# Kernel optimization log

Measured on AMD Instinct MI355X. Metric: run time of the kernel, lower is better.

Reference implementation:

```python
import jax, jax.numpy as jnp
import numpy as np

N_HEADS = 16


def _apply_rope(x, rope):
    # x: [B, H, N, Dh], rope: [B, N, Dh]; consecutive (even, odd) pairs form complex numbers
    xr, xi = x[..., 0::2], x[..., 1::2]              # [B,H,N,Dh/2]
    rr, ri = rope[:, None, :, 0::2], rope[:, None, :, 1::2]  # [B,1,N,Dh/2]
    or_ = xr * rr - xi * ri
    oi = xr * ri + xi * rr
    return jnp.stack([or_, oi], axis=-1).reshape(x.shape)


def setup_inputs() -> dict:
    key = jax.random.key(0)
    ks = jax.random.split(key, 8)
    B, N, D, Dh = 2, 2048, 2048, 128
    s = 0.02
    return {
        "x": jax.random.normal(ks[0], (B, N, D), jnp.float32),
        "q_rope": jax.random.normal(ks[1], (B, N, Dh), jnp.float32),
        "k_rope": jax.random.normal(ks[2], (B, N, Dh), jnp.float32),
        "Wq": jax.random.normal(ks[3], (D, D), jnp.float32) * s,
        "Wk": jax.random.normal(ks[4], (D, D), jnp.float32) * s,
        "Wv": jax.random.normal(ks[5], (D, D), jnp.float32) * s,
        "Wo": jax.random.normal(ks[6], (D, D), jnp.float32) * s,
        "bo": jax.random.normal(ks[7], (D,), jnp.float32) * s,
    }


def reference(x, q_rope, k_rope, Wq, Wk, Wv, Wo, bo):
    B, N, D = x.shape
    H = N_HEADS
    Dh = D // H
    # QKV projections (weights stored as [in, out])
    q = (x @ Wq).reshape(B, N, H, Dh).transpose(0, 2, 1, 3)  # [B,H,N,Dh]
    k = (x @ Wk).reshape(B, N, H, Dh).transpose(0, 2, 1, 3)
    v = (x @ Wv).reshape(B, N, H, Dh).transpose(0, 2, 1, 3)
    # NOTE: original scales q by d_head^-0.5 AND F.sdpa applies its default
    # 1/sqrt(d_head) scale again -> total score scale 1/d_head (faithful).
    q = q * (Dh ** -0.5)
    q = _apply_rope(q, q_rope)
    k = _apply_rope(k, k_rope)
    scores = jnp.einsum('bhnd,bhmd->bhnm', q, k) * (Dh ** -0.5)
    attn = jax.nn.softmax(scores, axis=-1)
    out = jnp.einsum('bhnm,bhmd->bhnd', attn, v)  # [B,H,N,Dh]
    out = out.transpose(0, 2, 1, 3).reshape(B, N, D)
    return out @ Wo + bo
```

## Files before the change

kernel.cpp:

```cpp
#include <hip/hip_runtime.h>
#include <hip/hip_bf16.h>
#include <stdint.h>


typedef __attribute__((ext_vector_type(4))) float f32x4;
typedef __attribute__((ext_vector_type(8))) short bf16x8;

__device__ __forceinline__ unsigned short f2bf(float f){
  unsigned u = __builtin_bit_cast(unsigned, f);
  u += 0x7FFFu + ((u >> 16) & 1u);
  return (unsigned short)(u >> 16);
}
__device__ __forceinline__ float bf2f(unsigned short h){
  unsigned u = ((unsigned)h) << 16;
  return __builtin_bit_cast(float, u);
}
__device__ __forceinline__ void gload16(const void* g, void* l){
  __builtin_amdgcn_global_load_lds((const __attribute__((address_space(1))) void*)g,
                                   (__attribute__((address_space(3))) void*)l, 16, 0, 0);
}

__global__ void k_cvt(const float* __restrict__ src, unsigned short* __restrict__ dst, int n4){
  int i = blockIdx.x * 256 + threadIdx.x;
  if (i >= n4) return;
  float4 v = ((const float4*)src)[i];
  unsigned long long pk = (unsigned long long)f2bf(v.x)
    | ((unsigned long long)f2bf(v.y) << 16)
    | ((unsigned long long)f2bf(v.z) << 32)
    | ((unsigned long long)f2bf(v.w) << 48);
  ((unsigned long long*)dst)[i] = pk;
}

__global__ void k_transpose_w(const float* __restrict__ W, unsigned short* __restrict__ WT){
  __shared__ float tile[64][65];
  int t = threadIdx.x;
  int cc = t & 63, rb = t >> 6;
  int bx = blockIdx.x * 64;
  int by = blockIdx.y * 64;
  #pragma unroll
  for (int i = 0; i < 16; i++){
    int r = rb + i * 4;
    tile[r][cc] = W[(size_t)(by + r) * 2048 + bx + cc];
  }
  __syncthreads();
  #pragma unroll
  for (int i = 0; i < 16; i++){
    int r = rb + i * 4;
    WT[(size_t)(bx + r) * 2048 + by + cc] = f2bf(tile[cc][r]);
  }
}

__global__ __launch_bounds__(256, 3) void k_gemm_qkv(
    const unsigned short* __restrict__ A,
    const unsigned short* __restrict__ Bt,
    unsigned short* __restrict__ Oq,
    unsigned short* __restrict__ Ok,
    unsigned short* __restrict__ Ov,
    const float* __restrict__ ropeq,
    const float* __restrict__ ropek)
{
  const int Kdim = 2048;
  __shared__ unsigned short As[128 * 64];
  __shared__ unsigned short Bs[128 * 64];
  const int tid = threadIdx.x;
  const int w = tid >> 6, l = tid & 63, g = l >> 4, c = l & 15;
  const int bm = blockIdx.x * 128, bn = blockIdx.y * 128;
  const int mw = (w >> 1) * 64, nw = (w & 1) * 64;
  f32x4 acc[4][4] = {};
  const int srow = l >> 3;
  const int sbyte = (((l & 7) ^ srow) << 4);
  const char* Ab = (const char*)A;
  const char* Bb = (const char*)Bt;
  char* AsB = (char*)As; char* BsB = (char*)Bs;

  for (int kt = 0; kt < Kdim; kt += 64){
    __syncthreads();
    #pragma unroll
    for (int j = 0; j < 4; j++){
      int chunk = w * 4 + j;
      int row = chunk * 8 + srow;
      gload16(Ab + ((size_t)(bm + row) * Kdim + kt) * 2 + sbyte, AsB + chunk * 1024);
      gload16(Bb + ((size_t)(bn + row) * Kdim + kt) * 2 + sbyte, BsB + chunk * 1024);
    }
    __syncthreads();
    #pragma unroll
    for (int kk = 0; kk < 2; kk++){
      bf16x8 av[4], bv[4];
      #pragma unroll
      for (int i = 0; i < 4; i++){
        int m = mw + i * 16 + c;
        av[i] = *(const bf16x8*)(AsB + m * 128 + ((kk * 64 + g * 16) ^ ((m & 7) << 4)));
        int n = nw + i * 16 + c;
        bv[i] = *(const bf16x8*)(BsB + n * 128 + ((kk * 64 + g * 16) ^ ((n & 7) << 4)));
      }
      #pragma unroll
      for (int i = 0; i < 4; i++)
        #pragma unroll
        for (int jj = 0; jj < 4; jj++)
          acc[i][jj] = __builtin_amdgcn_mfma_f32_16x16x32_bf16(av[i], bv[jj], acc[i][jj], 0, 0, 0);
    }
  }

  const int matsel = bn >> 11;
  const int hh = (bn >> 7) & 15;
  if (matsel < 2){
    unsigned short* O = matsel ? Ok : Oq;
    const float* rope = matsel ? ropek : ropeq;
    const float scale = matsel ? 1.0f : (1.0f / 128.0f);
    #pragma unroll
    for (int i = 0; i < 4; i++){
      int m0 = bm + mw + i * 16 + g * 4;
      #pragma unroll
      for (int jj = 0; jj < 4; jj++){
        int d = nw + jj * 16 + c;
        int dbase = d & ~1;
        int odd = d & 1;
        #pragma unroll
        for (int r = 0; r < 4; r++){
          int m = m0 + r;
          int b = m >> 11, tok = m & 2047;
          float v = acc[i][jj][r];
          float vp = __shfl_xor(v, 1);
          float2 rv = *(const float2*)(rope + (((size_t)(b * 2048 + tok)) << 7) + dbase);
          float xr = odd ? vp : v;
          float xi = odd ? v : vp;
          float res = odd ? (xr * rv.y + xi * rv.x) : (xr * rv.x - xi * rv.y);
          O[(((size_t)(b * 16 + hh) * 2048 + tok) << 7) + d] = f2bf(res * scale);
        }
      }
    }
  } else {
    #pragma unroll
    for (int i = 0; i < 4; i++){
      int m0 = bm + mw + i * 16 + g * 4;
      int b = m0 >> 11, tok0 = m0 & 2047;
      #pragma unroll
      for (int jj = 0; jj < 4; jj++){
        int d = nw + jj * 16 + c;
        unsigned long long pk = (unsigned long long)f2bf(acc[i][jj][0])
          | ((unsigned long long)f2bf(acc[i][jj][1]) << 16)
          | ((unsigned long long)f2bf(acc[i][jj][2]) << 32)
          | ((unsigned long long)f2bf(acc[i][jj][3]) << 48);
        *(unsigned long long*)(Ov + ((size_t)(b * 16 + hh) * 128 + d) * 2048 + tok0) = pk;
      }
    }
  }
}

__global__ __launch_bounds__(256, 3) void k_gemm_out(
    const unsigned short* __restrict__ A,
    const unsigned short* __restrict__ Bt,
    float* __restrict__ O,
    const float* __restrict__ bias)
{
  const int Kdim = 2048;
  __shared__ unsigned short As[128 * 64];
  __shared__ unsigned short Bs[128 * 64];
  const int tid = threadIdx.x;
  const int w = tid >> 6, l = tid & 63, g = l >> 4, c = l & 15;
  const int bm = blockIdx.x * 128, bn = blockIdx.y * 128;
  const int mw = (w >> 1) * 64, nw = (w & 1) * 64;
  f32x4 acc[4][4] = {};
  const int srow = l >> 3;
  const int sbyte = (((l & 7) ^ srow) << 4);
  const char* Ab = (const char*)A;
  const char* Bb = (const char*)Bt;
  char* AsB = (char*)As; char* BsB = (char*)Bs;

  for (int kt = 0; kt < Kdim; kt += 64){
    __syncthreads();
    #pragma unroll
    for (int j = 0; j < 4; j++){
      int chunk = w * 4 + j;
      int row = chunk * 8 + srow;
      gload16(Ab + ((size_t)(bm + row) * Kdim + kt) * 2 + sbyte, AsB + chunk * 1024);
      gload16(Bb + ((size_t)(bn + row) * Kdim + kt) * 2 + sbyte, BsB + chunk * 1024);
    }
    __syncthreads();
    #pragma unroll
    for (int kk = 0; kk < 2; kk++){
      bf16x8 av[4], bv[4];
      #pragma unroll
      for (int i = 0; i < 4; i++){
        int m = mw + i * 16 + c;
        av[i] = *(const bf16x8*)(AsB + m * 128 + ((kk * 64 + g * 16) ^ ((m & 7) << 4)));
        int n = nw + i * 16 + c;
        bv[i] = *(const bf16x8*)(BsB + n * 128 + ((kk * 64 + g * 16) ^ ((n & 7) << 4)));
      }
      #pragma unroll
      for (int i = 0; i < 4; i++)
        #pragma unroll
        for (int jj = 0; jj < 4; jj++)
          acc[i][jj] = __builtin_amdgcn_mfma_f32_16x16x32_bf16(av[i], bv[jj], acc[i][jj], 0, 0, 0);
    }
  }
  #pragma unroll
  for (int i = 0; i < 4; i++){
    int m0 = bm + mw + i * 16 + g * 4;
    #pragma unroll
    for (int jj = 0; jj < 4; jj++){
      int n = bn + nw + jj * 16 + c;
      float bv2 = bias[n];
      #pragma unroll
      for (int r = 0; r < 4; r++)
        O[(size_t)(m0 + r) * 2048 + n] = acc[i][jj][r] + bv2;
    }
  }
}

__global__ __launch_bounds__(256, 2) void k_attn(
    const unsigned short* __restrict__ Q,
    const unsigned short* __restrict__ Kg,
    const unsigned short* __restrict__ VT,
    unsigned short* __restrict__ Ao)
{
  __shared__ char sh[81920];
  char* PsB = sh + 65536;
  const int tid = threadIdx.x;
  const int w = tid >> 6, l = tid & 63, g = l >> 4, c = l & 15;
  const int qt = blockIdx.x, bh = blockIdx.y;
  const char* Qb = (const char*)(Q + (((size_t)bh * 2048 + qt * 128) << 7));
  const char* Kb = (const char*)(Kg + ((size_t)bh << 18));
  const char* Vb = (const char*)(VT + ((size_t)bh << 18));
  const int rsub = l >> 4;
  const int byte0 = (l & 15) << 4;
  const int drow = l >> 3;
  const int vbyte = (((l & 7) ^ drow) << 4);

  #pragma unroll
  for (int j = 0; j < 8; j++){
    int chunk = w * 8 + j;
    int row = chunk * 4 + rsub;
    gload16(Qb + (size_t)row * 256 + (byte0 ^ ((row & 7) << 4)), sh + chunk * 1024);
  }
  __syncthreads();
  bf16x8 qa[4][2];
  #pragma unroll
  for (int kk = 0; kk < 4; kk++)
    #pragma unroll
    for (int mf = 0; mf < 2; mf++){
      int q = w * 32 + mf * 16 + c;
      qa[kk][mf] = *(const bf16x8*)(sh + q * 256 + ((kk * 64 + g * 16) ^ ((q & 7) << 4)));
    }
  __syncthreads();

  auto stageKV = [&](int kv, int buf){
    char* Kc = sh + buf * 16384;
    char* Vc = sh + 32768 + buf * 16384;
    #pragma unroll
    for (int j = 0; j < 4; j++){
      int chunk = w * 4 + j;
      int row = chunk * 4 + rsub;
      gload16(Kb + (size_t)(kv * 64 + row) * 256 + (byte0 ^ ((row & 7) << 4)), Kc + chunk * 1024);
    }
    #pragma unroll
    for (int j = 0; j < 4; j++){
      int chunk = w * 4 + j;
      int d = chunk * 8 + drow;
      gload16(Vb + (size_t)d * 4096 + kv * 128 + vbyte, Vc + chunk * 1024);
    }
  };

  f32x4 oacc[2][8] = {};
  float lpart[2][4] = {};

  stageKV(0, 0);
  __syncthreads();

  for (int kv = 0; kv < 32; kv++){
    int cur = kv & 1;
    if (kv < 31) stageKV(kv + 1, cur ^ 1);
    char* Kc = sh + cur * 16384;
    char* Vc = sh + 32768 + cur * 16384;

    f32x4 sacc[2][4] = {};
    #pragma unroll
    for (int kk = 0; kk < 4; kk++){
      bf16x8 kbf[4];
      #pragma unroll
      for (int nf = 0; nf < 4; nf++){
        int kx = nf * 16 + c;
        kbf[nf] = *(const bf16x8*)(Kc + kx * 256 + ((kk * 64 + g * 16) ^ ((kx & 7) << 4)));
      }
      #pragma unroll
      for (int mf = 0; mf < 2; mf++)
        #pragma unroll
        for (int nf = 0; nf < 4; nf++)
          sacc[mf][nf] = __builtin_amdgcn_mfma_f32_16x16x32_bf16(qa[kk][mf], kbf[nf], sacc[mf][nf], 0, 0, 0);
    }

    #pragma unroll
    for (int mf = 0; mf < 2; mf++)
      #pragma unroll
      for (int nf = 0; nf < 4; nf++)
        #pragma unroll
        for (int r = 0; r < 4; r++){
          float pv = __expf(sacc[mf][nf][r]);
          sacc[mf][nf][r] = pv;
          lpart[mf][r] += pv;
        }

    #pragma unroll
    for (int mf = 0; mf < 2; mf++)
      #pragma unroll
      for (int nf = 0; nf < 4; nf++)
        #pragma unroll
        for (int r = 0; r < 4; r++){
          int q = w * 32 + mf * 16 + g * 4 + r;
          int key = nf * 16 + c;
          *(unsigned short*)(PsB + q * 128 + ((key * 2) ^ (((q >> 2) & 3) << 5))) = f2bf(sacc[mf][nf][r]);
        }
    __syncthreads();

    #pragma unroll
    for (int kk = 0; kk < 2; kk++){
      bf16x8 pa[2], vv[8];
      #pragma unroll
      for (int mf = 0; mf < 2; mf++){
        int q = w * 32 + mf * 16 + c;
        pa[mf] = *(const bf16x8*)(PsB + q * 128 + ((kk * 64 + g * 16) ^ (((q >> 2) & 3) << 5)));
      }
      #pragma unroll
      for (int df = 0; df < 8; df++){
        int d = df * 16 + c;
        vv[df] = *(const bf16x8*)(Vc + d * 128 + ((kk * 64 + g * 16) ^ ((d & 7) << 4)));
      }
      #pragma unroll
      for (int mf = 0; mf < 2; mf++)
        #pragma unroll
        for (int df = 0; df < 8; df++)
          oacc[mf][df] = __builtin_amdgcn_mfma_f32_16x16x32_bf16(pa[mf], vv[df], oacc[mf][df], 0, 0, 0);
    }
    __syncthreads();
  }

  int b = bh >> 4, h = bh & 15;
  #pragma unroll
  for (int mf = 0; mf < 2; mf++)
    #pragma unroll
    for (int r = 0; r < 4; r++){
      float s = lpart[mf][r];
      #pragma unroll
      for (int off = 1; off < 16; off <<= 1) s += __shfl_xor(s, off);
      float inv = 1.f / s;
      int qg = qt * 128 + w * 32 + mf * 16 + g * 4 + r;
      size_t rowbase = ((size_t)(b * 2048 + qg)) * 2048 + h * 128;
      #pragma unroll
      for (int df = 0; df < 8; df++)
        Ao[rowbase + df * 16 + c] = f2bf(oacc[mf][df][r] * inv);
    }
}

extern "C" void kernel_launch(void* const* d_in, const int* in_sizes, int n_in,
                              void* d_out, int out_size, void* d_ws, size_t ws_size,
                              hipStream_t stream){
  const float* x      = (const float*)d_in[0];
  const float* q_rope = (const float*)d_in[1];
  const float* k_rope = (const float*)d_in[2];
  const float* Wq     = (const float*)d_in[3];
  const float* Wk     = (const float*)d_in[4];
  const float* Wv     = (const float*)d_in[5];
  const float* Wo     = (const float*)d_in[6];
  const float* bo     = (const float*)d_in[7];
  char* ws = (char*)d_ws;
  unsigned short* xb  = (unsigned short*)(ws);
  unsigned short* wqT = (unsigned short*)(ws + 16777216);
  unsigned short* wkT = (unsigned short*)(ws + 25165824);
  unsigned short* wvT = (unsigned short*)(ws + 33554432);
  unsigned short* woT = (unsigned short*)(ws + 41943040);
  unsigned short* qb  = (unsigned short*)(ws + 50331648);
  unsigned short* kbf = (unsigned short*)(ws + 67108864);
  unsigned short* vt  = (unsigned short*)(ws + 83886080);
  unsigned short* ab  = (unsigned short*)(ws + 100663296);

  k_cvt<<<8192, 256, 0, stream>>>(x, xb, 2097152);
  dim3 tg(32, 32);
  k_transpose_w<<<tg, 256, 0, stream>>>(Wq, wqT);
  k_transpose_w<<<tg, 256, 0, stream>>>(Wk, wkT);
  k_transpose_w<<<tg, 256, 0, stream>>>(Wv, wvT);
  k_transpose_w<<<tg, 256, 0, stream>>>(Wo, woT);
  dim3 gq(32, 48);
  k_gemm_qkv<<<gq, 256, 0, stream>>>(xb, wqT, qb, kbf, vt, q_rope, k_rope);
  dim3 ga(16, 32);
  k_attn<<<ga, 256, 0, stream>>>(qb, kbf, vt, ab);
  dim3 go(32, 16);
  k_gemm_out<<<go, 256, 0, stream>>>(ab, woT, (float*)d_out, bo);
}
```

Baseline: 272.6 us.

## Remap blocks per XCD for L2 locality, merge weight transposes, add MFMA priority

Block indices in the QKV GEMM, output GEMM and attention kernels are remapped so that blocks sharing the same B-tile or head land on the same XCD (round-robin by index mod 8), aiming to improve L2 reuse. The four weight transpose launches are merged into one launch with a z dimension, which removes launch overhead. In attention, s_setprio raises wave priority around the MFMA sections so compute waves are favoured over waves issuing loads. The remapping relies on the hardware dispatching workgroups round-robin across XCDs, and the priority change may have no effect.

```diff
diff --git a/kernel.cpp b/kernel.cpp
--- a/kernel.cpp
+++ b/kernel.cpp
@@ -31,7 +31,11 @@
   ((unsigned long long*)dst)[i] = pk;
 }
 
-__global__ void k_transpose_w(const float* __restrict__ W, unsigned short* __restrict__ WT){
+__global__ void k_transpose_all(const float* __restrict__ W0, const float* __restrict__ W1,
+                                const float* __restrict__ W2, const float* __restrict__ W3,
+                                unsigned short* __restrict__ WT){
+  const float* W = (blockIdx.z == 0) ? W0 : (blockIdx.z == 1) ? W1 : (blockIdx.z == 2) ? W2 : W3;
+  unsigned short* dst = WT + (size_t)blockIdx.z * 4194304;
   __shared__ float tile[64][65];
   int t = threadIdx.x;
   int cc = t & 63, rb = t >> 6;
@@ -46,7 +50,7 @@
   #pragma unroll
   for (int i = 0; i < 16; i++){
     int r = rb + i * 4;
-    WT[(size_t)(bx + r) * 2048 + by + cc] = f2bf(tile[cc][r]);
+    dst[(size_t)(bx + r) * 2048 + by + cc] = f2bf(tile[cc][r]);
   }
 }
 
@@ -64,7 +68,10 @@
   __shared__ unsigned short Bs[128 * 64];
   const int tid = threadIdx.x;
   const int w = tid >> 6, l = tid & 63, g = l >> 4, c = l & 15;
-  const int bm = blockIdx.x * 128, bn = blockIdx.y * 128;
+  const int i0 = blockIdx.y * 32 + blockIdx.x;
+  const int xcd = i0 & 7, kb2 = i0 >> 3;
+  const int bm = (kb2 & 31) * 128;
+  const int bn = (xcd * 6 + (kb2 >> 5)) * 128;
   const int mw = (w >> 1) * 64, nw = (w & 1) * 64;
   f32x4 acc[4][4] = {};
   const int srow = l >> 3;
@@ -158,7 +165,10 @@
   __shared__ unsigned short Bs[128 * 64];
   const int tid = threadIdx.x;
   const int w = tid >> 6, l = tid & 63, g = l >> 4, c = l & 15;
-  const int bm = blockIdx.x * 128, bn = blockIdx.y * 128;
+  const int i0 = blockIdx.y * 32 + blockIdx.x;
+  const int xcd = i0 & 7, kb2 = i0 >> 3;
+  const int bm = (kb2 & 31) * 128;
+  const int bn = (xcd * 2 + (kb2 >> 5)) * 128;
   const int mw = (w >> 1) * 64, nw = (w & 1) * 64;
   f32x4 acc[4][4] = {};
   const int srow = l >> 3;
@@ -218,7 +228,10 @@
   char* PsB = sh + 65536;
   const int tid = threadIdx.x;
   const int w = tid >> 6, l = tid & 63, g = l >> 4, c = l & 15;
-  const int qt = blockIdx.x, bh = blockIdx.y;
+  const int i0 = blockIdx.y * 16 + blockIdx.x;
+  const int xcd = i0 & 7, kb2 = i0 >> 3;
+  const int bh = xcd * 4 + (kb2 >> 4);
+  const int qt = kb2 & 15;
   const char* Qb = (const char*)(Q + (((size_t)bh * 2048 + qt * 128) << 7));
   const char* Kb = (const char*)(Kg + ((size_t)bh << 18));
   const char* Vb = (const char*)(VT + ((size_t)bh << 18));
@@ -274,6 +287,7 @@
     char* Vc = sh + 32768 + cur * 16384;
 
     f32x4 sacc[2][4] = {};
+    __builtin_amdgcn_s_setprio(1);
     #pragma unroll
     for (int kk = 0; kk < 4; kk++){
       bf16x8 kbf[4];
@@ -288,6 +302,7 @@
         for (int nf = 0; nf < 4; nf++)
           sacc[mf][nf] = __builtin_amdgcn_mfma_f32_16x16x32_bf16(qa[kk][mf], kbf[nf], sacc[mf][nf], 0, 0, 0);
     }
+    __builtin_amdgcn_s_setprio(0);
 
     #pragma unroll
     for (int mf = 0; mf < 2; mf++)
@@ -312,6 +327,7 @@
         }
     __syncthreads();
 
+    __builtin_amdgcn_s_setprio(1);
     #pragma unroll
     for (int kk = 0; kk < 2; kk++){
       bf16x8 pa[2], vv[8];
@@ -331,6 +347,7 @@
         for (int df = 0; df < 8; df++)
           oacc[mf][df] = __builtin_amdgcn_mfma_f32_16x16x32_bf16(pa[mf], vv[df], oacc[mf][df], 0, 0, 0);
     }
+    __builtin_amdgcn_s_setprio(0);
     __syncthreads();
   }
 
@@ -365,8 +382,6 @@
   char* ws = (char*)d_ws;
   unsigned short* xb  = (unsigned short*)(ws);
   unsigned short* wqT = (unsigned short*)(ws + 16777216);
-  unsigned short* wkT = (unsigned short*)(ws + 25165824);
-  unsigned short* wvT = (unsigned short*)(ws + 33554432);
   unsigned short* woT = (unsigned short*)(ws + 41943040);
   unsigned short* qb  = (unsigned short*)(ws + 50331648);
   unsigned short* kbf = (unsigned short*)(ws + 67108864);
@@ -374,11 +389,8 @@
   unsigned short* ab  = (unsigned short*)(ws + 100663296);
 
   k_cvt<<<8192, 256, 0, stream>>>(x, xb, 2097152);
-  dim3 tg(32, 32);
-  k_transpose_w<<<tg, 256, 0, stream>>>(Wq, wqT);
-  k_transpose_w<<<tg, 256, 0, stream>>>(Wk, wkT);
-  k_transpose_w<<<tg, 256, 0, stream>>>(Wv, wvT);
-  k_transpose_w<<<tg, 256, 0, stream>>>(Wo, woT);
+  dim3 tg(32, 32, 4);
+  k_transpose_all<<<tg, 256, 0, stream>>>(Wq, Wk, Wv, Wo, wqT);
   dim3 gq(32, 48);
   k_gemm_qkv<<<gq, 256, 0, stream>>>(xb, wqT, qb, kbf, vt, q_rope, k_rope);
   dim3 ga(16, 32);
```

After: 279.8 us. 1.03x slower.
